# Performance work log

Measured on AMD Instinct MI355X. Metric: run time of the kernel, lower is better.

## Reference

```python
import jax, jax.numpy as jnp
import numpy as np

AXIS = 1          # reduction axis in the original input
KEEPDIM = False
INPUT_SHAPE = (4096, 2048)
B = 8             # leading grad-batch dim


def setup_inputs() -> dict:
    key = jax.random.key(0)
    k1, k2 = jax.random.split(key)
    grad_last = jax.random.normal(k1, (B, INPUT_SHAPE[0]), dtype=jnp.float32)
    indices = jax.random.randint(k2, (INPUT_SHAPE[0],), 0, INPUT_SHAPE[AXIS], dtype=jnp.int64)
    return {"grad_last": grad_last, "indices": indices}


def reference(grad_last, indices):
    # indices stored with a prepended grad-batch dim: [1, N]
    ind = indices[None, :]
    if not KEEPDIM:
        # unsqueeze at axis+1 (account for leading grad-batch dim)
        grad_last = jnp.expand_dims(grad_last, AXIS + 1)   # [B, N, 1]
        ind = jnp.expand_dims(ind, AXIS + 1)               # [1, N, 1]
    new_dim = INPUT_SHAPE[AXIS]
    # coord: iota along the reduced dim, broadcast against indices
    coord_shape = [1] * grad_last.ndim
    coord_shape[AXIS + 1] = new_dim
    coord = jnp.arange(new_dim).reshape(coord_shape)       # [1, 1, new_dim]
    mask = (coord == ind).astype(grad_last.dtype)          # [1, N, new_dim] -> broadcasts
    # one-hot scatter of grad to the argmax position: [B, N, new_dim]
    return mask * grad_last
```

## Files before the change

kernel.cpp:

```cpp
#include <hip/hip_runtime.h>


#define ROWS_PER_B 4096
#define NEWDIM     2048
#define F4_PER_ROW (NEWDIM / 4)
#define NTHREADS   524288
#define ITERS      32

typedef float f32x4 __attribute__((ext_vector_type(4)));

__global__ __launch_bounds__(256)
void ReduceMaxGrad_53833120088407_kernel(const float* __restrict__ grad,
                                         const int*  __restrict__ indices,
                                         float*      __restrict__ out) {
    const int gtid     = blockIdx.x * 256 + threadIdx.x;
    const int c4       = gtid & (F4_PER_ROW - 1);
    const int row_base = gtid >> 9;
    const int c4x4     = c4 << 2;

    f32x4* o = (f32x4*)out + gtid;

    int   idx = indices[row_base & (ROWS_PER_B - 1)];
    float g   = grad[row_base];

#pragma unroll
    for (int i = 0; i < ITERS; ++i) {
        int   nidx = 0;
        float ng   = 0.0f;
        if (i + 1 < ITERS) {
            const int nrow = (i + 1) * 1024 + row_base;
            nidx = indices[nrow & (ROWS_PER_B - 1)];
            ng   = grad[nrow];
        }
        const int c = idx - c4x4;
        f32x4 v;
        v.x = (c == 0) ? g : 0.0f;
        v.y = (c == 1) ? g : 0.0f;
        v.z = (c == 2) ? g : 0.0f;
        v.w = (c == 3) ? g : 0.0f;
        o[(size_t)i * NTHREADS] = v;
        idx = nidx; g = ng;
    }
}

extern "C" void kernel_launch(void* const* d_in, const int* in_sizes, int n_in,
                              void* d_out, int out_size, void* d_ws, size_t ws_size,
                              hipStream_t stream) {
    const float* grad    = (const float*)d_in[0];
    const int*   indices = (const int*)d_in[1];
    float*       out     = (float*)d_out;

    ReduceMaxGrad_53833120088407_kernel<<<dim3(2048), dim3(256), 0, stream>>>(
        grad, indices, out);
}
```

Baseline: 257.2 us.

## Replace dense one-hot write with memset plus sparse scatter kernel

Drops the kernel that builds every output element from a compare and select, and replaces it with a driver memset of the whole output followed by a small kernel that writes one gradient value per row at its index. The aim is to let the memset's fill path handle the bulk zero writes and cut per-element ALU work. This adds a second launch and a dependency between the memset and the scatter, and it still writes the full 256MB output once. It also adds an unused n_rows variable that reads in_sizes.

```diff
diff --git a/kernel.cpp b/kernel.cpp
--- a/kernel.cpp
+++ b/kernel.cpp
@@ -3,44 +3,16 @@
 
 #define ROWS_PER_B 4096
 #define NEWDIM     2048
-#define F4_PER_ROW (NEWDIM / 4)
-#define NTHREADS   524288
-#define ITERS      32
 
-typedef float f32x4 __attribute__((ext_vector_type(4)));
-
-__global__ __launch_bounds__(256)
-void ReduceMaxGrad_53833120088407_kernel(const float* __restrict__ grad,
-                                         const int*  __restrict__ indices,
-                                         float*      __restrict__ out) {
-    const int gtid     = blockIdx.x * 256 + threadIdx.x;
-    const int c4       = gtid & (F4_PER_ROW - 1);
-    const int row_base = gtid >> 9;
-    const int c4x4     = c4 << 2;
-
-    f32x4* o = (f32x4*)out + gtid;
-
-    int   idx = indices[row_base & (ROWS_PER_B - 1)];
-    float g   = grad[row_base];
-
-#pragma unroll
-    for (int i = 0; i < ITERS; ++i) {
-        int   nidx = 0;
-        float ng   = 0.0f;
-        if (i + 1 < ITERS) {
-            const int nrow = (i + 1) * 1024 + row_base;
-            nidx = indices[nrow & (ROWS_PER_B - 1)];
-            ng   = grad[nrow];
-        }
-        const int c = idx - c4x4;
-        f32x4 v;
-        v.x = (c == 0) ? g : 0.0f;
-        v.y = (c == 1) ? g : 0.0f;
-        v.z = (c == 2) ? g : 0.0f;
-        v.w = (c == 3) ? g : 0.0f;
-        o[(size_t)i * NTHREADS] = v;
-        idx = nidx; g = ng;
-    }
+__global__ __launch_bounds__(512)
+void ReduceMaxGrad_53833120088407_scatter(const float* __restrict__ grad,
+                                          const int*  __restrict__ indices,
+                                          float*      __restrict__ out) {
+    const int t = blockIdx.x * 512 + threadIdx.x;
+    const int i = t & (ROWS_PER_B - 1);
+    const int idx = indices[i];
+    const float g = grad[t];
+    out[(size_t)t * NEWDIM + idx] = g;
 }
 
 extern "C" void kernel_launch(void* const* d_in, const int* in_sizes, int n_in,
@@ -50,6 +22,9 @@
     const int*   indices = (const int*)d_in[1];
     float*       out     = (float*)d_out;
 
-    ReduceMaxGrad_53833120088407_kernel<<<dim3(2048), dim3(256), 0, stream>>>(
+    hipMemsetAsync(d_out, 0, (size_t)out_size, stream);
+
+    const int n_rows = in_sizes[0] * (n_in > 0 ? 1 : 1);
+    ReduceMaxGrad_53833120088407_scatter<<<dim3(32768 / 512), dim3(512), 0, stream>>>(
         grad, indices, out);
 }
```

Measured after the change: 228.8 us. 1.12x faster.
